# Optimization experiments

Hardware: AMD Instinct MI355X
Metric: run time of the kernel (lower is better)

The kernel has to match this reference:

```python
import jax, jax.numpy as jnp
import numpy as np

N_NODES = 32768
N_EDGES = 524288
HID = 128


def _linear_params(key, fan_in, fan_out):
    kw, kb = jax.random.split(key)
    bound = 1.0 / np.sqrt(fan_in)
    w = jax.random.uniform(kw, (fan_in, fan_out), jnp.float32, -bound, bound)
    b = jax.random.uniform(kb, (fan_out,), jnp.float32, -bound, bound)
    return w, b


def setup_inputs() -> dict:
    key = jax.random.key(0)
    ks = jax.random.split(key, 8)
    x = jax.random.normal(ks[0], (N_NODES, HID), jnp.float32)
    edge_attr = jax.random.normal(ks[1], (N_EDGES, HID), jnp.float32)
    edges = jax.random.randint(ks[2], (2, N_EDGES), 0, N_NODES, jnp.int32)
    w1, b1 = _linear_params(ks[3], 3 * HID, HID)      # message_fn layer 1
    w2, b2 = _linear_params(ks[4], HID, HID)          # message_fn layer 2
    wu1, bu1 = _linear_params(ks[5], HID, 2 * HID)    # update_fn layer 1
    wu2, bu2 = _linear_params(ks[6], 2 * HID, HID)    # update_fn layer 2
    return {"x": x, "edge_attr": edge_attr, "edges": edges,
            "w1": w1, "b1": b1, "w2": w2, "b2": b2,
            "wu1": wu1, "bu1": bu1, "wu2": wu2, "bu2": bu2}


def reference(x, edge_attr, edges, w1, b1, w2, b2, wu1, bu1, wu2, bu2):
    n_nodes = x.shape[0]
    send, recv = edges[0], edges[1]
    # gather endpoint features and concat with edge attributes: [E, 3*HID]
    ea = jnp.concatenate([x[send], x[recv], edge_attr], axis=-1)
    # per-edge message MLP (Linear-SiLU-Linear-SiLU)
    h = jax.nn.silu(ea @ w1 + b1)
    msg = jax.nn.silu(h @ w2 + b2)                    # [E, HID]
    # scatter-mean into receiving nodes
    sums = jax.ops.segment_sum(msg, recv, num_segments=n_nodes)
    counts = jax.ops.segment_sum(jnp.ones((msg.shape[0],), msg.dtype), recv,
                                 num_segments=n_nodes)
    aggr = sums / jnp.maximum(counts, 1.0)[:, None]
    # residual (input_size == hidden_size -> Identity) + update MLP
    xo = x + aggr
    xo = xo + (jax.nn.silu(xo @ wu1 + bu1) @ wu2 + bu2)
    return xo, msg
```

## Files before the change

### kernel.cpp

```cpp
#include <hip/hip_runtime.h>
#include <hip/hip_bf16.h>

#define NN 32768
#define NE 524288
#define HID 128

typedef unsigned short u16;
typedef unsigned int u32;
typedef __bf16 bf16x8 __attribute__((ext_vector_type(8)));
typedef float f32x4 __attribute__((ext_vector_type(4)));

__device__ __forceinline__ u16 f2bf(float f) {
  union { float f; unsigned u; } v; v.f = f;
  return (u16)((v.u + 0x7fffu + ((v.u >> 16) & 1u)) >> 16);
}
__device__ __forceinline__ float silu_f(float v) {
  return v * __builtin_amdgcn_rcpf(1.f + __expf(-v));
}

__device__ __forceinline__ void gld16(const void* g, void* l) {
  __builtin_amdgcn_global_load_lds(
      (const __attribute__((address_space(1))) u32*)g,
      (__attribute__((address_space(3))) u32*)l, 16, 0, 0);
}

__global__ __launch_bounds__(256) void prep_k(
    const float* __restrict__ x, const float* __restrict__ w1,
    const float* __restrict__ w2, const float* __restrict__ wu1,
    const float* __restrict__ wu2,
    u16* __restrict__ xb, u16* __restrict__ w1Ts, u16* __restrict__ w2Ts,
    u16* __restrict__ wu1T, u16* __restrict__ wu2T, int* __restrict__ cnt)
{
  int i = blockIdx.x * 256 + threadIdx.x;
  xb[i] = f2bf(x[i]);
  if (i < NN) cnt[i] = 0;
  if (i < 3 * 128 * 128) {
    int j = i & 7, qs = (i >> 3) & 15, c = (i >> 7) & 127, s = i >> 14;
    int k = s * 128 + ((qs ^ (c & 7)) << 3) + j;
    w1Ts[i] = f2bf(w1[k * 128 + c]);
  }
  if (i < 128 * 128) {
    int j = i & 7, qs = (i >> 3) & 15, c = i >> 7;
    int k = ((qs ^ (c & 7)) << 3) + j;
    w2Ts[i] = f2bf(w2[k * 128 + c]);
  }
  if (i < 256 * 128) { int c = i >> 7, k = i & 127; wu1T[i] = f2bf(wu1[k * 256 + c]); }
  if (i < 128 * 256) { int c = i >> 8, k = i & 255; wu2T[i] = f2bf(wu2[k * 128 + c]); }
}

__global__ __launch_bounds__(256) void count_k(const int* __restrict__ recv,
                                               int* __restrict__ cnt)
{
  int e = blockIdx.x * 256 + threadIdx.x;
  atomicAdd(&cnt[recv[e]], 1);
}

__global__ __launch_bounds__(1024) void scan_k(const int* __restrict__ cnt,
                                               int* __restrict__ off,
                                               int* __restrict__ cursor)
{
  __shared__ int part[1024];
  const int tid = threadIdx.x;
  const int base = tid * 32;
  int v[32];
  int s = 0;
  #pragma unroll
  for (int j = 0; j < 32; ++j) { v[j] = cnt[base + j]; s += v[j]; }
  part[tid] = s;
  __syncthreads();
  #pragma unroll 1
  for (int d = 1; d < 1024; d <<= 1) {
    int t = (tid >= d) ? part[tid - d] : 0;
    __syncthreads();
    part[tid] += t;
    __syncthreads();
  }
  int ex = part[tid] - s;
  #pragma unroll
  for (int j = 0; j < 32; ++j) {
    off[base + j] = ex;
    cursor[base + j] = ex;
    ex += v[j];
  }
  if (tid == 1023) off[NN] = ex;
}

__global__ __launch_bounds__(256) void scatter_k(const int* __restrict__ recv,
                                                 int* __restrict__ cursor,
                                                 int* __restrict__ eperm)
{
  int e = blockIdx.x * 256 + threadIdx.x;
  int r = recv[e];
  int pos = atomicAdd(&cursor[r], 1);
  eperm[pos] = e;
}

__global__ __launch_bounds__(512, 4) void edge_mlp(
    const u16* __restrict__ xb, const float* __restrict__ eattr,
    const int* __restrict__ send, const int* __restrict__ recv,
    const u16* __restrict__ w1Ts, const float* __restrict__ b1,
    const u16* __restrict__ w2Ts, const float* __restrict__ b2,
    float* __restrict__ msg_out)
{
  __shared__ u16 sA[128 * 128];
  __shared__ u16 sB[128 * 128];

  const int tid  = threadIdx.x;
  const int lane = tid & 63;
  const int w    = tid >> 6;
  const int wr   = w >> 1;
  const int wc   = w & 1;
  const int fr   = lane & 15;
  const int fkq  = lane >> 4;
  const int orow = fkq * 4;
  const int e0   = blockIdx.x * 128;

  const int lrow4 = lane >> 4;
  const int schk  = lane & 15;

  int nds[4], ndr[4];
  #pragma unroll
  for (int i = 0; i < 4; ++i) {
    int e = e0 + w * 16 + i * 4 + lrow4;
    nds[i] = send[e];
    ndr[i] = recv[e];
  }

  f32x4 acc[2][4];
  #pragma unroll
  for (int m = 0; m < 2; ++m)
    #pragma unroll
    for (int n = 0; n < 4; ++n)
      #pragma unroll
      for (int r = 0; r < 4; ++r) acc[m][n][r] = 0.f;

  #pragma unroll
  for (int s = 0; s < 3; ++s) {
    if (s < 2) {
      #pragma unroll
      for (int i = 0; i < 4; ++i) {
        int rloc = w * 16 + i * 4 + lrow4;
        int node = (s == 0) ? nds[i] : ndr[i];
        gld16(xb + ((size_t)node << 7) + ((schk ^ (rloc & 7)) << 3),
              sA + ((w * 16 + i * 4) << 7));
      }
    } else {
      #pragma unroll
      for (int i = 0; i < 4; ++i) {
        int rloc = w * 16 + i * 4 + lrow4;
        int gchk = schk ^ (rloc & 7);
        const float4* p = reinterpret_cast<const float4*>(
            eattr + ((size_t)(e0 + rloc) << 7) + (gchk << 3));
        float4 v0 = p[0], v1 = p[1];
        uint4 d;
        d.x = (unsigned)f2bf(v0.x) | ((unsigned)f2bf(v0.y) << 16);
        d.y = (unsigned)f2bf(v0.z) | ((unsigned)f2bf(v0.w) << 16);
        d.z = (unsigned)f2bf(v1.x) | ((unsigned)f2bf(v1.y) << 16);
        d.w = (unsigned)f2bf(v1.z) | ((unsigned)f2bf(v1.w) << 16);
        *reinterpret_cast<uint4*>(sA + (rloc << 7) + (schk << 3)) = d;
      }
    }
    #pragma unroll
    for (int i = 0; i < 4; ++i) {
      gld16(w1Ts + ((size_t)s << 14) + ((w * 16 + i * 4) << 7) + (lane << 3),
            sB + ((w * 16 + i * 4) << 7));
    }
    __syncthreads();
    #pragma unroll
    for (int kk = 0; kk < 4; ++kk) {
      bf16x8 aF[2], bF[4];
      #pragma unroll
      for (int m = 0; m < 2; ++m) {
        int row = wr * 32 + m * 16 + fr;
        int ch = (kk * 4 + fkq) ^ (row & 7);
        aF[m] = __builtin_bit_cast(bf16x8,
            *reinterpret_cast<const uint4*>(sA + (row << 7) + (ch << 3)));
      }
      #pragma unroll
      for (int n = 0; n < 4; ++n) {
        int c = wc * 64 + n * 16 + fr;
        int ch = (kk * 4 + fkq) ^ (c & 7);
        bF[n] = __builtin_bit_cast(bf16x8,
            *reinterpret_cast<const uint4*>(sB + (c << 7) + (ch << 3)));
      }
      #pragma unroll
      for (int m = 0; m < 2; ++m)
        #pragma unroll
        for (int n = 0; n < 4; ++n)
          acc[m][n] = __builtin_amdgcn_mfma_f32_16x16x32_bf16(aF[m], bF[n], acc[m][n], 0, 0, 0);
    }
    __syncthreads();
  }

  #pragma unroll
  for (int n = 0; n < 4; ++n) {
    int c = wc * 64 + n * 16 + fr;
    float bb = b1[c];
    #pragma unroll
    for (int m = 0; m < 2; ++m) {
      #pragma unroll
      for (int r = 0; r < 4; ++r) {
        int row = wr * 32 + m * 16 + orow + r;
        sA[(row << 7) + (((c >> 3) ^ (row & 7)) << 3) + (c & 7)] =
            f2bf(silu_f(acc[m][n][r] + bb));
        acc[m][n][r] = 0.f;
      }
    }
  }
  #pragma unroll
  for (int i = 0; i < 4; ++i) {
    gld16(w2Ts + ((w * 16 + i * 4) << 7) + (lane << 3),
          sB + ((w * 16 + i * 4) << 7));
  }
  __syncthreads();

  #pragma unroll
  for (int kk = 0; kk < 4; ++kk) {
    bf16x8 aF[2], bF[4];
    #pragma unroll
    for (int m = 0; m < 2; ++m) {
      int row = wr * 32 + m * 16 + fr;
      int ch = (kk * 4 + fkq) ^ (row & 7);
      aF[m] = __builtin_bit_cast(bf16x8,
          *reinterpret_cast<const uint4*>(sA + (row << 7) + (ch << 3)));
    }
    #pragma unroll
    for (int n = 0; n < 4; ++n) {
      int c = wc * 64 + n * 16 + fr;
      int ch = (kk * 4 + fkq) ^ (c & 7);
      bF[n] = __builtin_bit_cast(bf16x8,
          *reinterpret_cast<const uint4*>(sB + (c << 7) + (ch << 3)));
    }
    #pragma unroll
    for (int m = 0; m < 2; ++m)
      #pragma unroll
      for (int n = 0; n < 4; ++n)
        acc[m][n] = __builtin_amdgcn_mfma_f32_16x16x32_bf16(aF[m], bF[n], acc[m][n], 0, 0, 0);
  }

  #pragma unroll
  for (int m = 0; m < 2; ++m) {
    #pragma unroll
    for (int r = 0; r < 4; ++r) {
      int e = e0 + wr * 32 + m * 16 + orow + r;
      #pragma unroll
      for (int n = 0; n < 4; ++n) {
        int c = wc * 64 + n * 16 + fr;
        msg_out[(size_t)e * HID + c] = silu_f(acc[m][n][r] + b2[c]);
      }
    }
  }
}

__global__ __launch_bounds__(256) void agg_k(
    const float* __restrict__ msg, const int* __restrict__ off,
    const int* __restrict__ eperm, const float* __restrict__ x,
    float* __restrict__ xin, u16* __restrict__ xob)
{
  const int wid = threadIdx.x >> 6, lane = threadIdx.x & 63;
  const int n = blockIdx.x * 4 + wid;
  const int j0 = off[n], j1 = off[n + 1];
  float ax = 0.f, ay = 0.f;
  int j = j0;
  for (; j + 1 < j1; j += 2) {
    int ea = eperm[j], eb = eperm[j + 1];
    float2 va = reinterpret_cast<const float2*>(msg + (size_t)ea * HID)[lane];
    float2 vb = reinterpret_cast<const float2*>(msg + (size_t)eb * HID)[lane];
    ax += va.x + vb.x;
    ay += va.y + vb.y;
  }
  if (j < j1) {
    int ea = eperm[j];
    float2 va = reinterpret_cast<const float2*>(msg + (size_t)ea * HID)[lane];
    ax += va.x; ay += va.y;
  }
  float inv = (j1 > j0) ? 1.f / (float)(j1 - j0) : 1.f;
  float2 xv = reinterpret_cast<const float2*>(x + (size_t)n * HID)[lane];
  float x0 = xv.x + ax * inv, x1 = xv.y + ay * inv;
  reinterpret_cast<float2*>(xin + (size_t)n * HID)[lane] = make_float2(x0, x1);
  reinterpret_cast<unsigned*>(xob)[n * 64 + lane] =
      (unsigned)f2bf(x0) | ((unsigned)f2bf(x1) << 16);
}

__global__ __launch_bounds__(256) void mlp1_k(
    const u16* __restrict__ xob, const u16* __restrict__ wu1T,
    const float* __restrict__ bu1, u16* __restrict__ t)
{
  __shared__ u16 sB[256][40];
  const int tid = threadIdx.x, lane = tid & 63, wid = tid >> 6;
  const int wr = wid >> 1, wc = wid & 1;
  const int fr = lane & 15, fk = (lane >> 4) * 8, orow = (lane >> 4) * 4;
  const int n0 = blockIdx.x * 64;

  f32x4 acc[2][8];
  #pragma unroll
  for (int m = 0; m < 2; ++m)
    #pragma unroll
    for (int n = 0; n < 8; ++n)
      #pragma unroll
      for (int r = 0; r < 4; ++r) acc[m][n][r] = 0.f;

  #pragma unroll 1
  for (int kk = 0; kk < 4; ++kk) {
    #pragma unroll
    for (int it = 0; it < 4; ++it) {
      int chunk = tid + it * 256;
      int c = chunk >> 2, q = chunk & 3;
      *reinterpret_cast<uint4*>(&sB[c][q * 8]) =
          *reinterpret_cast<const uint4*>(wu1T + c * 128 + kk * 32 + q * 8);
    }
    __syncthreads();
    bf16x8 aF[2], bF[8];
    #pragma unroll
    for (int m = 0; m < 2; ++m)
      aF[m] = __builtin_bit_cast(bf16x8, *reinterpret_cast<const uint4*>(
          xob + (size_t)(n0 + wr * 32 + m * 16 + fr) * HID + kk * 32 + fk));
    #pragma unroll
    for (int n = 0; n < 8; ++n)
      bF[n] = __builtin_bit_cast(bf16x8,
          *reinterpret_cast<const uint4*>(&sB[wc * 128 + n * 16 + fr][fk]));
    #pragma unroll
    for (int m = 0; m < 2; ++m)
      #pragma unroll
      for (int n = 0; n < 8; ++n)
        acc[m][n] = __builtin_amdgcn_mfma_f32_16x16x32_bf16(aF[m], bF[n], acc[m][n], 0, 0, 0);
    __syncthreads();
  }
  #pragma unroll
  for (int n = 0; n < 8; ++n) {
    int col = wc * 128 + n * 16 + fr;
    float bb = bu1[col];
    #pragma unroll
    for (int m = 0; m < 2; ++m) {
      int row = n0 + wr * 32 + m * 16 + orow;
      #pragma unroll
      for (int r = 0; r < 4; ++r)
        t[(size_t)(row + r) * 256 + col] = f2bf(silu_f(acc[m][n][r] + bb));
    }
  }
}

__global__ __launch_bounds__(256) void mlp2_k(
    const u16* __restrict__ t, const u16* __restrict__ wu2T,
    const float* __restrict__ bu2, const float* __restrict__ xin,
    float* __restrict__ xo)
{
  __shared__ u16 sB[128][40];
  const int tid = threadIdx.x, lane = tid & 63, wid = tid >> 6;
  const int wr = wid >> 1, wc = wid & 1;
  const int fr = lane & 15, fk = (lane >> 4) * 8, orow = (lane >> 4) * 4;
  const int n0 = blockIdx.x * 64;

  f32x4 acc[2][4];
  #pragma unroll
  for (int m = 0; m < 2; ++m)
    #pragma unroll
    for (int n = 0; n < 4; ++n)
      #pragma unroll
      for (int r = 0; r < 4; ++r) acc[m][n][r] = 0.f;

  #pragma unroll 1
  for (int kk = 0; kk < 8; ++kk) {
    #pragma unroll
    for (int it = 0; it < 2; ++it) {
      int chunk = tid + it * 256;
      int c = chunk >> 2, q = chunk & 3;
      *reinterpret_cast<uint4*>(&sB[c][q * 8]) =
          *reinterpret_cast<const uint4*>(wu2T + c * 256 + kk * 32 + q * 8);
    }
    __syncthreads();
    bf16x8 aF[2], bF[4];
    #pragma unroll
    for (int m = 0; m < 2; ++m)
      aF[m] = __builtin_bit_cast(bf16x8, *reinterpret_cast<const uint4*>(
          t + (size_t)(n0 + wr * 32 + m * 16 + fr) * 256 + kk * 32 + fk));
    #pragma unroll
    for (int n = 0; n < 4; ++n)
      bF[n] = __builtin_bit_cast(bf16x8,
          *reinterpret_cast<const uint4*>(&sB[wc * 64 + n * 16 + fr][fk]));
    #pragma unroll
    for (int m = 0; m < 2; ++m)
      #pragma unroll
      for (int n = 0; n < 4; ++n)
        acc[m][n] = __builtin_amdgcn_mfma_f32_16x16x32_bf16(aF[m], bF[n], acc[m][n], 0, 0, 0);
    __syncthreads();
  }
  #pragma unroll
  for (int m = 0; m < 2; ++m) {
    #pragma unroll
    for (int r = 0; r < 4; ++r) {
      int gn = n0 + wr * 32 + m * 16 + orow + r;
      #pragma unroll
      for (int n = 0; n < 4; ++n) {
        int col = wc * 64 + n * 16 + fr;
        xo[(size_t)gn * HID + col] =
            xin[(size_t)gn * HID + col] + acc[m][n][r] + bu2[col];
      }
    }
  }
}

extern "C" void kernel_launch(void* const* d_in, const int* in_sizes, int n_in,
                              void* d_out, int out_size, void* d_ws, size_t ws_size,
                              hipStream_t stream)
{
  (void)in_sizes; (void)n_in; (void)out_size; (void)ws_size;
  const float* x     = (const float*)d_in[0];
  const float* eattr = (const float*)d_in[1];
  const int*   edges = (const int*)d_in[2];
  const float* w1  = (const float*)d_in[3];
  const float* b1  = (const float*)d_in[4];
  const float* w2  = (const float*)d_in[5];
  const float* b2  = (const float*)d_in[6];
  const float* wu1 = (const float*)d_in[7];
  const float* bu1 = (const float*)d_in[8];
  const float* wu2 = (const float*)d_in[9];
  const float* bu2 = (const float*)d_in[10];

  float* xo  = (float*)d_out;
  float* msg = xo + (size_t)NN * HID;

  char* p = (char*)d_ws;
  u16* xb    = (u16*)p; p += (size_t)NN * HID * 2;
  u16* w1Ts  = (u16*)p; p += 384 * 128 * 2;
  u16* w2Ts  = (u16*)p; p += 128 * 128 * 2;
  u16* wu1T  = (u16*)p; p += 256 * 128 * 2;
  u16* wu2T  = (u16*)p; p += 128 * 256 * 2;
  u16* xob   = (u16*)p; p += (size_t)NN * HID * 2;
  u16* tbuf  = (u16*)p; p += (size_t)NN * 256 * 2;
  float* xin = (float*)p; p += (size_t)NN * HID * 4;
  int* cnt    = (int*)p; p += (size_t)NN * 4;
  int* off    = (int*)p; p += (size_t)(NN + 64) * 4;
  int* cursor = (int*)p; p += (size_t)NN * 4;
  int* eperm  = (int*)p; p += (size_t)NE * 4;

  const int* send = edges;
  const int* recv = edges + NE;

  prep_k<<<NN * HID / 256, 256, 0, stream>>>(x, w1, w2, wu1, wu2,
                                             xb, w1Ts, w2Ts, wu1T, wu2T, cnt);
  count_k<<<NE / 256, 256, 0, stream>>>(recv, cnt);
  scan_k<<<1, 1024, 0, stream>>>(cnt, off, cursor);
  scatter_k<<<NE / 256, 256, 0, stream>>>(recv, cursor, eperm);
  edge_mlp<<<NE / 128, 512, 0, stream>>>(xb, eattr, send, recv,
                                         w1Ts, b1, w2Ts, b2, msg);
  agg_k<<<NN / 4, 256, 0, stream>>>(msg, off, eperm, x, xin, xob);
  mlp1_k<<<NN / 64, 256, 0, stream>>>(xob, wu1T, bu1, tbuf);
  mlp2_k<<<NN / 64, 256, 0, stream>>>(tbuf, wu2T, bu2, xin, xo);
}
```

Measured before the change: 339.4 us.

## Fuse scatter-mean into edge MLP via receiver-sorted edges and segmented atomics

The edge MLP now processes edges in receiver-sorted order (via eperm) and reduces each block's messages per receiver in shared memory, then atomically adds the partial sums into a global sums buffer. This removes the separate agg_k pass that re-read the full fp32 message tensor. The edge kernel is also restructured with double-buffered LDS (four 32KB buffers, occupancy hint lowered to 2), explicit waitcnt/sched barriers, MFMA priority bumps, and overlapped prefetch of edge attributes and weights. Count is folded into prep_k with memsets replacing the zeroing, and xin is recomputed in mlp2_k instead of stored. The costs are float atomics on sums (non-deterministic ordering), summing bf16-rounded messages, which loses precision, and scattered msg writes and eattr reads through the permutation.

Result: slower. 390.9 us (+15.2%).

```diff
diff --git a/kernel.cpp b/kernel.cpp
--- a/kernel.cpp
+++ b/kernel.cpp
@@ -11,11 +11,16 @@
 typedef float f32x4 __attribute__((ext_vector_type(4)));
 
 __device__ __forceinline__ u16 f2bf(float f) {
-  union { float f; unsigned u; } v; v.f = f;
-  return (u16)((v.u + 0x7fffu + ((v.u >> 16) & 1u)) >> 16);
+  return __builtin_bit_cast(u16, (__bf16)f);
 }
 __device__ __forceinline__ float silu_f(float v) {
   return v * __builtin_amdgcn_rcpf(1.f + __expf(-v));
+}
+__device__ __forceinline__ bf16x8 cvt8(float4 a, float4 b) {
+  bf16x8 r;
+  r[0] = (__bf16)a.x; r[1] = (__bf16)a.y; r[2] = (__bf16)a.z; r[3] = (__bf16)a.w;
+  r[4] = (__bf16)b.x; r[5] = (__bf16)b.y; r[6] = (__bf16)b.z; r[7] = (__bf16)b.w;
+  return r;
 }
 
 __device__ __forceinline__ void gld16(const void* g, void* l) {
@@ -24,16 +29,28 @@
       (__attribute__((address_space(3))) u32*)l, 16, 0, 0);
 }
 
+#define WV(N)  do { asm volatile("s_waitcnt vmcnt(" #N ")" ::: "memory"); \
+                    __builtin_amdgcn_sched_barrier(0); } while (0)
+#define WVL(N) do { asm volatile("s_waitcnt vmcnt(" #N ") lgkmcnt(0)" ::: "memory"); \
+                    __builtin_amdgcn_sched_barrier(0); } while (0)
+#define WL()   do { asm volatile("s_waitcnt lgkmcnt(0)" ::: "memory"); \
+                    __builtin_amdgcn_sched_barrier(0); } while (0)
+__device__ __forceinline__ void bar() {
+  __builtin_amdgcn_sched_barrier(0);
+  __builtin_amdgcn_s_barrier();
+  __builtin_amdgcn_sched_barrier(0);
+}
+
 __global__ __launch_bounds__(256) void prep_k(
     const float* __restrict__ x, const float* __restrict__ w1,
     const float* __restrict__ w2, const float* __restrict__ wu1,
-    const float* __restrict__ wu2,
+    const float* __restrict__ wu2, const int* __restrict__ recv,
     u16* __restrict__ xb, u16* __restrict__ w1Ts, u16* __restrict__ w2Ts,
     u16* __restrict__ wu1T, u16* __restrict__ wu2T, int* __restrict__ cnt)
 {
   int i = blockIdx.x * 256 + threadIdx.x;
   xb[i] = f2bf(x[i]);
-  if (i < NN) cnt[i] = 0;
+  if (i < NE) atomicAdd(&cnt[recv[i]], 1);
   if (i < 3 * 128 * 128) {
     int j = i & 7, qs = (i >> 3) & 15, c = (i >> 7) & 127, s = i >> 14;
     int k = s * 128 + ((qs ^ (c & 7)) << 3) + j;
@@ -46,13 +63,6 @@
   }
   if (i < 256 * 128) { int c = i >> 7, k = i & 127; wu1T[i] = f2bf(wu1[k * 256 + c]); }
   if (i < 128 * 256) { int c = i >> 8, k = i & 255; wu2T[i] = f2bf(wu2[k * 128 + c]); }
-}
-
-__global__ __launch_bounds__(256) void count_k(const int* __restrict__ recv,
-                                               int* __restrict__ cnt)
-{
-  int e = blockIdx.x * 256 + threadIdx.x;
-  atomicAdd(&cnt[recv[e]], 1);
 }
 
 __global__ __launch_bounds__(1024) void scan_k(const int* __restrict__ cnt,
@@ -95,15 +105,50 @@
   eperm[pos] = e;
 }
 
-__global__ __launch_bounds__(512, 4) void edge_mlp(
+__device__ __forceinline__ void cslice(const u16* __restrict__ bufA,
+                                       const u16* __restrict__ bufB,
+                                       f32x4 (&acc)[2][4],
+                                       int wr, int wc, int fr, int fkq)
+{
+  #pragma unroll
+  for (int kk = 0; kk < 4; ++kk) {
+    bf16x8 aF[2], bF[4];
+    #pragma unroll
+    for (int m = 0; m < 2; ++m) {
+      int row = wr * 32 + m * 16 + fr;
+      int ch = (kk * 4 + fkq) ^ (row & 7);
+      aF[m] = __builtin_bit_cast(bf16x8,
+          *reinterpret_cast<const uint4*>(bufA + (row << 7) + (ch << 3)));
+    }
+    #pragma unroll
+    for (int n = 0; n < 4; ++n) {
+      int c = wc * 64 + n * 16 + fr;
+      int ch = (kk * 4 + fkq) ^ (c & 7);
+      bF[n] = __builtin_bit_cast(bf16x8,
+          *reinterpret_cast<const uint4*>(bufB + (c << 7) + (ch << 3)));
+    }
+    __builtin_amdgcn_s_setprio(1);
+    #pragma unroll
+    for (int m = 0; m < 2; ++m)
+      #pragma unroll
+      for (int n = 0; n < 4; ++n)
+        acc[m][n] = __builtin_amdgcn_mfma_f32_16x16x32_bf16(aF[m], bF[n], acc[m][n], 0, 0, 0);
+    __builtin_amdgcn_s_setprio(0);
+  }
+}
+
+__global__ __launch_bounds__(512, 2) void edge_mlp(
     const u16* __restrict__ xb, const float* __restrict__ eattr,
     const int* __restrict__ send, const int* __restrict__ recv,
+    const int* __restrict__ eperm,
     const u16* __restrict__ w1Ts, const float* __restrict__ b1,
     const u16* __restrict__ w2Ts, const float* __restrict__ b2,
-    float* __restrict__ msg_out)
-{
-  __shared__ u16 sA[128 * 128];
-  __shared__ u16 sB[128 * 128];
+    float* __restrict__ msg_out, float* __restrict__ sums)
+{
+  __shared__ u16 sA0[128 * 128];
+  __shared__ u16 sA1[128 * 128];
+  __shared__ u16 sB0[128 * 128];
+  __shared__ u16 sB1[128 * 128];
 
   const int tid  = threadIdx.x;
   const int lane = tid & 63;
@@ -114,17 +159,53 @@
   const int fkq  = lane >> 4;
   const int orow = fkq * 4;
   const int e0   = blockIdx.x * 128;
-
   const int lrow4 = lane >> 4;
   const int schk  = lane & 15;
 
-  int nds[4], ndr[4];
+  int eo[4], ns[4], nr[4];
+  #pragma unroll
+  for (int i = 0; i < 4; ++i) eo[i] = eperm[e0 + w * 16 + i * 4 + lrow4];
+  #pragma unroll
+  for (int i = 0; i < 4; ++i) { ns[i] = send[eo[i]]; nr[i] = recv[eo[i]]; }
+  float b1v[4], b2v[4];
+  #pragma unroll
+  for (int n = 0; n < 4; ++n) {
+    b1v[n] = b1[wc * 64 + n * 16 + fr];
+    b2v[n] = b2[wc * 64 + n * 16 + fr];
+  }
+  WV(0);
+
   #pragma unroll
   for (int i = 0; i < 4; ++i) {
-    int e = e0 + w * 16 + i * 4 + lrow4;
-    nds[i] = send[e];
-    ndr[i] = recv[e];
-  }
+    int rloc = w * 16 + i * 4 + lrow4;
+    gld16(xb + ((size_t)ns[i] << 7) + ((schk ^ (rloc & 7)) << 3),
+          sA0 + ((w * 16 + i * 4) << 7));
+  }
+  #pragma unroll
+  for (int i = 0; i < 4; ++i)
+    gld16(w1Ts + ((w * 16 + i * 4) << 7) + (lane << 3),
+          sB0 + ((w * 16 + i * 4) << 7));
+  __builtin_amdgcn_sched_barrier(0);
+  #pragma unroll
+  for (int i = 0; i < 4; ++i) {
+    int rloc = w * 16 + i * 4 + lrow4;
+    gld16(xb + ((size_t)nr[i] << 7) + ((schk ^ (rloc & 7)) << 3),
+          sA1 + ((w * 16 + i * 4) << 7));
+  }
+  #pragma unroll
+  for (int i = 0; i < 4; ++i)
+    gld16(w1Ts + 16384 + ((w * 16 + i * 4) << 7) + (lane << 3),
+          sB1 + ((w * 16 + i * 4) << 7));
+  __builtin_amdgcn_sched_barrier(0);
+  float4 ea0[4], ea1[4];
+  #pragma unroll
+  for (int i = 0; i < 4; ++i) {
+    int rloc = w * 16 + i * 4 + lrow4;
+    const float* ep = eattr + ((size_t)eo[i] << 7) + ((schk ^ (rloc & 7)) << 3);
+    ea0[i] = *reinterpret_cast<const float4*>(ep);
+    ea1[i] = *reinterpret_cast<const float4*>(ep + 4);
+  }
+  __builtin_amdgcn_sched_barrier(0);
 
   f32x4 acc[2][4];
   #pragma unroll
@@ -134,152 +215,105 @@
       #pragma unroll
       for (int r = 0; r < 4; ++r) acc[m][n][r] = 0.f;
 
-  #pragma unroll
-  for (int s = 0; s < 3; ++s) {
-    if (s < 2) {
-      #pragma unroll
-      for (int i = 0; i < 4; ++i) {
-        int rloc = w * 16 + i * 4 + lrow4;
-        int node = (s == 0) ? nds[i] : ndr[i];
-        gld16(xb + ((size_t)node << 7) + ((schk ^ (rloc & 7)) << 3),
-              sA + ((w * 16 + i * 4) << 7));
+  WV(16); bar();
+  cslice(sA0, sB0, acc, wr, wc, fr, fkq);
+  WV(8); bar();
+
+  #pragma unroll
+  for (int i = 0; i < 4; ++i)
+    gld16(w1Ts + 32768 + ((w * 16 + i * 4) << 7) + (lane << 3),
+          sB0 + ((w * 16 + i * 4) << 7));
+  #pragma unroll
+  for (int i = 0; i < 4; ++i) {
+    int rloc = w * 16 + i * 4 + lrow4;
+    *reinterpret_cast<uint4*>(sA0 + (rloc << 7) + (schk << 3)) =
+        __builtin_bit_cast(uint4, cvt8(ea0[i], ea1[i]));
+  }
+  cslice(sA1, sB1, acc, wr, wc, fr, fkq);
+  WVL(0); bar();
+
+  #pragma unroll
+  for (int i = 0; i < 4; ++i)
+    gld16(w2Ts + ((w * 16 + i * 4) << 7) + (lane << 3),
+          sB1 + ((w * 16 + i * 4) << 7));
+  cslice(sA0, sB0, acc, wr, wc, fr, fkq);
+
+  #pragma unroll
+  for (int n = 0; n < 4; ++n) {
+    #pragma unroll
+    for (int m = 0; m < 2; ++m)
+      #pragma unroll
+      for (int r = 0; r < 4; ++r) {
+        int c = wc * 64 + n * 16 + fr;
+        int row = wr * 32 + m * 16 + orow + r;
+        sA1[(row << 7) + (((c >> 3) ^ (row & 7)) << 3) + (c & 7)] =
+            f2bf(silu_f(acc[m][n][r] + b1v[n]));
+        acc[m][n][r] = 0.f;
       }
-    } else {
-      #pragma unroll
-      for (int i = 0; i < 4; ++i) {
-        int rloc = w * 16 + i * 4 + lrow4;
-        int gchk = schk ^ (rloc & 7);
-        const float4* p = reinterpret_cast<const float4*>(
-            eattr + ((size_t)(e0 + rloc) << 7) + (gchk << 3));
-        float4 v0 = p[0], v1 = p[1];
-        uint4 d;
-        d.x = (unsigned)f2bf(v0.x) | ((unsigned)f2bf(v0.y) << 16);
-        d.y = (unsigned)f2bf(v0.z) | ((unsigned)f2bf(v0.w) << 16);
-        d.z = (unsigned)f2bf(v1.x) | ((unsigned)f2bf(v1.y) << 16);
-        d.w = (unsigned)f2bf(v1.z) | ((unsigned)f2bf(v1.w) << 16);
-        *reinterpret_cast<uint4*>(sA + (rloc << 7) + (schk << 3)) = d;
-      }
-    }
-    #pragma unroll
-    for (int i = 0; i < 4; ++i) {
-      gld16(w1Ts + ((size_t)s << 14) + ((w * 16 + i * 4) << 7) + (lane << 3),
-            sB + ((w * 16 + i * 4) << 7));
-    }
-    __syncthreads();
-    #pragma unroll
-    for (int kk = 0; kk < 4; ++kk) {
-      bf16x8 aF[2], bF[4];
-      #pragma unroll
-      for (int m = 0; m < 2; ++m) {
-        int row = wr * 32 + m * 16 + fr;
-        int ch = (kk * 4 + fkq) ^ (row & 7);
-        aF[m] = __builtin_bit_cast(bf16x8,
-            *reinterpret_cast<const uint4*>(sA + (row << 7) + (ch << 3)));
-      }
+  }
+  WVL(0); bar();
+  cslice(sA1, sB1, acc, wr, wc, fr, fkq);
+
+  int* snid = reinterpret_cast<int*>(sA0);
+  #pragma unroll
+  for (int i = 0; i < 4; ++i) snid[w * 16 + i * 4 + lrow4] = nr[i];
+
+  #pragma unroll
+  for (int m = 0; m < 2; ++m) {
+    int eg[4];
+    #pragma unroll
+    for (int r = 0; r < 4; ++r)
+      eg[r] = eperm[e0 + wr * 32 + m * 16 + orow + r];
+    #pragma unroll
+    for (int r = 0; r < 4; ++r) {
+      int row = wr * 32 + m * 16 + orow + r;
+      float* mp = msg_out + ((size_t)eg[r] << 7);
       #pragma unroll
       for (int n = 0; n < 4; ++n) {
         int c = wc * 64 + n * 16 + fr;
-        int ch = (kk * 4 + fkq) ^ (c & 7);
-        bF[n] = __builtin_bit_cast(bf16x8,
-            *reinterpret_cast<const uint4*>(sB + (c << 7) + (ch << 3)));
+        float v = silu_f(acc[m][n][r] + b2v[n]);
+        mp[c] = v;
+        sB0[(row << 7) + (((c >> 3) ^ (row & 7)) << 3) + (c & 7)] = f2bf(v);
       }
-      #pragma unroll
-      for (int m = 0; m < 2; ++m)
-        #pragma unroll
-        for (int n = 0; n < 4; ++n)
-          acc[m][n] = __builtin_amdgcn_mfma_f32_16x16x32_bf16(aF[m], bF[n], acc[m][n], 0, 0, 0);
-    }
-    __syncthreads();
-  }
-
-  #pragma unroll
-  for (int n = 0; n < 4; ++n) {
-    int c = wc * 64 + n * 16 + fr;
-    float bb = b1[c];
-    #pragma unroll
-    for (int m = 0; m < 2; ++m) {
-      #pragma unroll
-      for (int r = 0; r < 4; ++r) {
-        int row = wr * 32 + m * 16 + orow + r;
-        sA[(row << 7) + (((c >> 3) ^ (row & 7)) << 3) + (c & 7)] =
-            f2bf(silu_f(acc[m][n][r] + bb));
-        acc[m][n][r] = 0.f;
+    }
+  }
+  WL(); bar();
+
+  {
+    const int col = tid & 127, q = tid >> 7;
+    const int row0 = q * 32;
+    float s = 0.f;
+    int cur = snid[row0];
+    #pragma unroll 1
+    for (int r = 0; r < 32; ++r) {
+      int row = row0 + r;
+      u16 hv = sB0[(row << 7) + (((col >> 3) ^ (row & 7)) << 3) + (col & 7)];
+      s += __builtin_bit_cast(float, (u32)hv << 16);
+      int nxt = (r < 31) ? snid[row + 1] : -1;
+      if (nxt != cur) {
+        atomicAdd(sums + (size_t)cur * HID + col, s);
+        s = 0.f;
+        cur = nxt;
       }
     }
   }
-  #pragma unroll
-  for (int i = 0; i < 4; ++i) {
-    gld16(w2Ts + ((w * 16 + i * 4) << 7) + (lane << 3),
-          sB + ((w * 16 + i * 4) << 7));
-  }
-  __syncthreads();
-
-  #pragma unroll
-  for (int kk = 0; kk < 4; ++kk) {
-    bf16x8 aF[2], bF[4];
-    #pragma unroll
-    for (int m = 0; m < 2; ++m) {
-      int row = wr * 32 + m * 16 + fr;
-      int ch = (kk * 4 + fkq) ^ (row & 7);
-      aF[m] = __builtin_bit_cast(bf16x8,
-          *reinterpret_cast<const uint4*>(sA + (row << 7) + (ch << 3)));
-    }
-    #pragma unroll
-    for (int n = 0; n < 4; ++n) {
-      int c = wc * 64 + n * 16 + fr;
-      int ch = (kk * 4 + fkq) ^ (c & 7);
-      bF[n] = __builtin_bit_cast(bf16x8,
-          *reinterpret_cast<const uint4*>(sB + (c << 7) + (ch << 3)));
-    }
-    #pragma unroll
-    for (int m = 0; m < 2; ++m)
-      #pragma unroll
-      for (int n = 0; n < 4; ++n)
-        acc[m][n] = __builtin_amdgcn_mfma_f32_16x16x32_bf16(aF[m], bF[n], acc[m][n], 0, 0, 0);
-  }
-
-  #pragma unroll
-  for (int m = 0; m < 2; ++m) {
-    #pragma unroll
-    for (int r = 0; r < 4; ++r) {
-      int e = e0 + wr * 32 + m * 16 + orow + r;
-      #pragma unroll
-      for (int n = 0; n < 4; ++n) {
-        int c = wc * 64 + n * 16 + fr;
-        msg_out[(size_t)e * HID + c] = silu_f(acc[m][n][r] + b2[c]);
-      }
-    }
-  }
-}
-
-__global__ __launch_bounds__(256) void agg_k(
-    const float* __restrict__ msg, const int* __restrict__ off,
-    const int* __restrict__ eperm, const float* __restrict__ x,
-    float* __restrict__ xin, u16* __restrict__ xob)
-{
-  const int wid = threadIdx.x >> 6, lane = threadIdx.x & 63;
-  const int n = blockIdx.x * 4 + wid;
-  const int j0 = off[n], j1 = off[n + 1];
-  float ax = 0.f, ay = 0.f;
-  int j = j0;
-  for (; j + 1 < j1; j += 2) {
-    int ea = eperm[j], eb = eperm[j + 1];
-    float2 va = reinterpret_cast<const float2*>(msg + (size_t)ea * HID)[lane];
-    float2 vb = reinterpret_cast<const float2*>(msg + (size_t)eb * HID)[lane];
-    ax += va.x + vb.x;
-    ay += va.y + vb.y;
-  }
-  if (j < j1) {
-    int ea = eperm[j];
-    float2 va = reinterpret_cast<const float2*>(msg + (size_t)ea * HID)[lane];
-    ax += va.x; ay += va.y;
-  }
-  float inv = (j1 > j0) ? 1.f / (float)(j1 - j0) : 1.f;
-  float2 xv = reinterpret_cast<const float2*>(x + (size_t)n * HID)[lane];
-  float x0 = xv.x + ax * inv, x1 = xv.y + ay * inv;
-  reinterpret_cast<float2*>(xin + (size_t)n * HID)[lane] = make_float2(x0, x1);
-  reinterpret_cast<unsigned*>(xob)[n * 64 + lane] =
-      (unsigned)f2bf(x0) | ((unsigned)f2bf(x1) << 16);
+}
+
+__global__ __launch_bounds__(256) void xin_k(
+    const float* __restrict__ x, const float* __restrict__ sums,
+    const int* __restrict__ cnt, u16* __restrict__ xob)
+{
+  int idx = blockIdx.x * 256 + threadIdx.x;
+  int node = idx >> 5;
+  float inv = 1.f / fmaxf((float)cnt[node], 1.f);
+  float4 xv = reinterpret_cast<const float4*>(x)[idx];
+  float4 sv = reinterpret_cast<const float4*>(sums)[idx];
+  float o0 = xv.x + sv.x * inv, o1 = xv.y + sv.y * inv;
+  float o2 = xv.z + sv.z * inv, o3 = xv.w + sv.w * inv;
+  uint2 wv;
+  wv.x = (u32)f2bf(o0) | ((u32)f2bf(o1) << 16);
+  wv.y = (u32)f2bf(o2) | ((u32)f2bf(o3) << 16);
+  reinterpret_cast<uint2*>(xob)[idx] = wv;
 }
 
 __global__ __launch_bounds__(256) void mlp1_k(
@@ -342,7 +376,8 @@
 
 __global__ __launch_bounds__(256) void mlp2_k(
     const u16* __restrict__ t, const u16* __restrict__ wu2T,
-    const float* __restrict__ bu2, const float* __restrict__ xin,
+    const float* __restrict__ bu2, const float* __restrict__ x,
+    const float* __restrict__ sums, const int* __restrict__ cnt,
     float* __restrict__ xo)
 {
   __shared__ u16 sB[128][40];
@@ -390,11 +425,12 @@
     #pragma unroll
     for (int r = 0; r < 4; ++r) {
       int gn = n0 + wr * 32 + m * 16 + orow + r;
+      float inv = 1.f / fmaxf((float)cnt[gn], 1.f);
       #pragma unroll
       for (int n = 0; n < 4; ++n) {
         int col = wc * 64 + n * 16 + fr;
-        xo[(size_t)gn * HID + col] =
-            xin[(size_t)gn * HID + col] + acc[m][n][r] + bu2[col];
+        float xi = x[(size_t)gn * HID + col] + sums[(size_t)gn * HID + col] * inv;
+        xo[(size_t)gn * HID + col] = xi + acc[m][n][r] + bu2[col];
       }
     }
   }
@@ -428,7 +464,7 @@
   u16* wu2T  = (u16*)p; p += 128 * 256 * 2;
   u16* xob   = (u16*)p; p += (size_t)NN * HID * 2;
   u16* tbuf  = (u16*)p; p += (size_t)NN * 256 * 2;
-  float* xin = (float*)p; p += (size_t)NN * HID * 4;
+  float* sums = (float*)p; p += (size_t)NN * HID * 4;
   int* cnt    = (int*)p; p += (size_t)NN * 4;
   int* off    = (int*)p; p += (size_t)(NN + 64) * 4;
   int* cursor = (int*)p; p += (size_t)NN * 4;
@@ -437,14 +473,15 @@
   const int* send = edges;
   const int* recv = edges + NE;
 
-  prep_k<<<NN * HID / 256, 256, 0, stream>>>(x, w1, w2, wu1, wu2,
+  hipMemsetAsync(cnt, 0, (size_t)NN * 4, stream);
+  hipMemsetAsync(sums, 0, (size_t)NN * HID * 4, stream);
+  prep_k<<<NN * HID / 256, 256, 0, stream>>>(x, w1, w2, wu1, wu2, recv,
                                              xb, w1Ts, w2Ts, wu1T, wu2T, cnt);
-  count_k<<<NE / 256, 256, 0, stream>>>(recv, cnt);
   scan_k<<<1, 1024, 0, stream>>>(cnt, off, cursor);
   scatter_k<<<NE / 256, 256, 0, stream>>>(recv, cursor, eperm);
-  edge_mlp<<<NE / 128, 512, 0, stream>>>(xb, eattr, send, recv,
-                                         w1Ts, b1, w2Ts, b2, msg);
-  agg_k<<<NN / 4, 256, 0, stream>>>(msg, off, eperm, x, xin, xob);
+  edge_mlp<<<NE / 128, 512, 0, stream>>>(xb, eattr, send, recv, eperm,
+                                         w1Ts, b1, w2Ts, b2, msg, sums);
+  xin_k<<<NN * HID / 4 / 256, 256, 0, stream>>>(x, sums, cnt, xob);
   mlp1_k<<<NN / 64, 256, 0, stream>>>(xob, wu1T, bu1, tbuf);
-  mlp2_k<<<NN / 64, 256, 0, stream>>>(tbuf, wu2T, bu2, xin, xo);
-}
+  mlp2_k<<<NN / 64, 256, 0, stream>>>(tbuf, wu2T, bu2, x, sums, cnt, xo);
+}
```
